# Performance work log

Measured on AMD Instinct MI355X. Metric: run time of the kernel, lower is better.

The kernel has to match this reference:

```python
import jax, jax.numpy as jnp
import numpy as np

EPS = 1e-7


def setup_inputs() -> dict:
    key = jax.random.key(0)
    k1, k2, k3 = jax.random.split(key, 3)
    B, Nt, Nv, D = 64, 128, 256, 512
    text_feats = jax.random.normal(k1, (B, Nt, D), dtype=jnp.float32)
    visual_feats = jax.random.normal(k2, (B, Nv, D), dtype=jnp.float32)
    attention_mask = jax.random.randint(k3, (B, Nt), 0, 2, dtype=jnp.int32)
    return {"text_feats": text_feats, "visual_feats": visual_feats,
            "attention_mask": attention_mask}


def _l2norm(x):
    return x / jnp.clip(jnp.linalg.norm(x, axis=-1, keepdims=True), 1e-12)


def reference(text_feats, visual_feats, attention_mask):
    # Normalize token features (F.normalize along D)
    t = _l2norm(text_feats)            # (B, Nt, D)
    v = _l2norm(visual_feats)          # (B, Nv, D)
    # All-pairs token similarities: (B, B, Nt, Nv)
    token_sims = jnp.einsum('itd,jvd->ijtv', t, v)
    # Max over visual tokens -> (B, B, Nt)
    max_sims = jnp.max(token_sims, axis=3)
    # Masked mean over text tokens -> (B, B)
    mask = attention_mask.astype(jnp.float32)[:, None, :]   # (B, 1, Nt) broadcasts over pairs
    masked_sum = jnp.sum(max_sims * mask, axis=2)            # (B, B)
    valid = jnp.clip(jnp.sum(mask, axis=2), EPS)             # (B, 1)
    clip_sims = masked_sum / valid                           # (B, B)
    # Symmetric InfoNCE on the diagonal
    B = clip_sims.shape[0]
    diag = jnp.arange(B)
    losses_t2v = -jax.nn.log_softmax(clip_sims, axis=1)[diag, diag]
    losses_v2t = -jax.nn.log_softmax(clip_sims.T, axis=1)[diag, diag]
    contrastive_loss = jnp.mean(losses_t2v + losses_v2t) / 2.0
    # Regularization: keep negative token sims near zero
    neg_sims = jnp.clip(token_sims, -20.0, 0.0)
    reg_loss = 0.15 * jnp.mean(neg_sims ** 2)
    return contrastive_loss + reg_loss
```

## Files before the change

### kernel.cpp

```cpp
#include <hip/hip_runtime.h>
#include <hip/hip_bf16.h>

#define BB 64
#define NT 128
#define NV 256
#define DD 512
#define BKB 128
#define EPSF 1e-7f

typedef __attribute__((ext_vector_type(8))) int i32x8;
typedef __attribute__((ext_vector_type(4))) int i32x4;
typedef __attribute__((ext_vector_type(4))) float f32x4;

__device__ __forceinline__ void glds16(const uchar* g, uchar* l) {
    __builtin_amdgcn_global_load_lds(
        (const __attribute__((address_space(1))) unsigned int*)g,
        (__attribute__((address_space(3))) unsigned int*)l, 16, 0, 0);
}

__global__ __launch_bounds__(256) void k_normalize(
    const float* __restrict__ tf, const float* __restrict__ vf,
    uchar* __restrict__ tn, uchar* __restrict__ vn,
    float* __restrict__ reg_sum) {
    if (blockIdx.x == 0 && threadIdx.x == 0) *reg_sum = 0.0f;
    const int w = threadIdx.x >> 6, l = threadIdx.x & 63;
    const int row = blockIdx.x * 4 + w;
    const float* src;
    uchar* dst;
    if (row < BB * NT) {
        src = tf + (size_t)row * DD;
        dst = tn + (size_t)row * DD;
    } else {
        int r = row - BB * NT;
        src = vf + (size_t)r * DD;
        dst = vn + (size_t)r * DD;
    }
    float4 x0 = ((const float4*)src)[l * 2];
    float4 x1 = ((const float4*)src)[l * 2 + 1];
    float ss = x0.x * x0.x + x0.y * x0.y + x0.z * x0.z + x0.w * x0.w
             + x1.x * x1.x + x1.y * x1.y + x1.z * x1.z + x1.w * x1.w;
    #pragma unroll
    for (int off = 32; off; off >>= 1) ss += __shfl_xor(ss, off, 64);
    float scale = 1.0f / fmaxf(sqrtf(ss), 1e-12f);
    int p0 = __builtin_amdgcn_cvt_pk_fp8_f32(x0.x * scale, x0.y * scale, 0, 0);
    p0 = __builtin_amdgcn_cvt_pk_fp8_f32(x0.z * scale, x0.w * scale, p0, 1);
    int p1 = __builtin_amdgcn_cvt_pk_fp8_f32(x1.x * scale, x1.y * scale, 0, 0);
    p1 = __builtin_amdgcn_cvt_pk_fp8_f32(x1.z * scale, x1.w * scale, p1, 1);
    ((uint2*)dst)[l] = make_uint2((unsigned)p0, (unsigned)p1);
}

__global__ __launch_bounds__(512, 2) void k_gemm(
    const uchar* __restrict__ tn, const uchar* __restrict__ vn,
    const int* __restrict__ mask,
    float* __restrict__ clip_sims, float* __restrict__ reg_sum) {
    __shared__ uchar sT0[NT * BKB];
    __shared__ uchar sT1[NT * BKB];
    __shared__ uchar sV0[NV * BKB];
    __shared__ uchar sV1[NV * BKB];
    __shared__ float maxbuf[NT][4];
    __shared__ float redw[8];
    __shared__ float c0[2], c1[2];

    const int i = blockIdx.x, j = blockIdx.y;
    const int tid = threadIdx.x;
    const int l = tid & 63, w = tid >> 6;
    const int wr = w >> 2, wc = w & 3;
    const int m15 = l & 15, q = l >> 4;

    const uchar* tbase = tn + (size_t)i * NT * DD;
    const uchar* vbase = vn + (size_t)j * NV * DD;

    int t_off[2], v_off[4];
    #pragma unroll
    for (int s = 0; s < 2; ++s) {
        int f = s * 512 + tid;
        int r = f >> 3, p = f & 7, g = (p - r) & 7;
        t_off[s] = r * DD + g * 16;
    }
    #pragma unroll
    for (int s = 0; s < 4; ++s) {
        int f = s * 512 + tid;
        int r = f >> 3, p = f & 7, g = (p - r) & 7;
        v_off[s] = r * DD + g * 16;
    }

    int a_b0[4], a_b1[4], b_b0[4], b_b1[4];
    #pragma unroll
    for (int rt = 0; rt < 4; ++rt) {
        int row = wr * 64 + rt * 16 + m15;
        a_b0[rt] = row * BKB + (((2 * q + row) & 7) * 16);
        a_b1[rt] = row * BKB + (((2 * q + 1 + row) & 7) * 16);
    }
    #pragma unroll
    for (int ct = 0; ct < 4; ++ct) {
        int row = wc * 64 + ct * 16 + m15;
        b_b0[ct] = row * BKB + (((2 * q + row) & 7) * 16);
        b_b1[ct] = row * BKB + (((2 * q + 1 + row) & 7) * 16);
    }

    f32x4 acc[4][4];
    #pragma unroll
    for (int rt = 0; rt < 4; ++rt)
        #pragma unroll
        for (int ct = 0; ct < 4; ++ct) acc[rt][ct] = (f32x4){0.f, 0.f, 0.f, 0.f};

    auto stage = [&](uchar* dT, uchar* dV, int kk) {
        #pragma unroll
        for (int s = 0; s < 2; ++s)
            glds16(tbase + t_off[s] + kk, dT + (s * 512 + tid) * 16);
        #pragma unroll
        for (int s = 0; s < 4; ++s)
            glds16(vbase + v_off[s] + kk, dV + (s * 512 + tid) * 16);
    };
    auto compute = [&](const uchar* bT, const uchar* bV) {
        i32x8 bf[4];
        #pragma unroll
        for (int ct = 0; ct < 4; ++ct) {
            i32x4 lo = *(const i32x4*)(bV + b_b0[ct]);
            i32x4 hi = *(const i32x4*)(bV + b_b1[ct]);
            bf[ct] = (i32x8){lo.x, lo.y, lo.z, lo.w, hi.x, hi.y, hi.z, hi.w};
        }
        #pragma unroll
        for (int rt = 0; rt < 4; ++rt) {
            i32x4 lo = *(const i32x4*)(bT + a_b0[rt]);
            i32x4 hi = *(const i32x4*)(bT + a_b1[rt]);
            i32x8 a = (i32x8){lo.x, lo.y, lo.z, lo.w, hi.x, hi.y, hi.z, hi.w};
            #pragma unroll
            for (int ct = 0; ct < 4; ++ct)
                acc[rt][ct] = __builtin_amdgcn_mfma_scale_f32_16x16x128_f8f6f4(
                    a, bf[ct], acc[rt][ct],
                    0 , 0 ,
                    0, 127 , 0, 127 );
        }
    };

    stage(sT0, sV0, 0);
    stage(sT1, sV1, 1 * BKB);

    asm volatile("s_waitcnt vmcnt(6)" ::: "memory");
    __builtin_amdgcn_s_barrier();
    asm volatile("" ::: "memory");
    compute(sT0, sV0);
    asm volatile("" ::: "memory");
    __builtin_amdgcn_s_barrier();
    stage(sT0, sV0, 2 * BKB);

    asm volatile("s_waitcnt vmcnt(6)" ::: "memory");
    __builtin_amdgcn_s_barrier();
    asm volatile("" ::: "memory");
    compute(sT1, sV1);
    asm volatile("" ::: "memory");
    __builtin_amdgcn_s_barrier();
    stage(sT1, sV1, 3 * BKB);

    asm volatile("s_waitcnt vmcnt(6)" ::: "memory");
    __builtin_amdgcn_s_barrier();
    asm volatile("" ::: "memory");
    compute(sT0, sV0);
    asm volatile("" ::: "memory");
    __builtin_amdgcn_s_barrier();

    asm volatile("s_waitcnt vmcnt(0)" ::: "memory");
    __builtin_amdgcn_s_barrier();
    asm volatile("" ::: "memory");
    compute(sT1, sV1);

    float rp = 0.0f;
    #pragma unroll
    for (int rt = 0; rt < 4; ++rt)
        #pragma unroll
        for (int ct = 0; ct < 4; ++ct)
            #pragma unroll
            for (int r = 0; r < 4; ++r) {
                float m = fminf(acc[rt][ct][r], 0.0f);
                rp = fmaf(m, m, rp);
            }

    #pragma unroll
    for (int rt = 0; rt < 4; ++rt)
        #pragma unroll
        for (int r = 0; r < 4; ++r) {
            float m = acc[rt][0][r];
            #pragma unroll
            for (int ct = 1; ct < 4; ++ct) m = fmaxf(m, acc[rt][ct][r]);
            #pragma unroll
            for (int msk = 1; msk < 16; msk <<= 1)
                m = fmaxf(m, __shfl_xor(m, msk, 64));
            if (m15 == 0)
                maxbuf[wr * 64 + rt * 16 + q * 4 + r][wc] = m;
        }

    #pragma unroll
    for (int off = 32; off; off >>= 1) rp += __shfl_down(rp, off, 64);
    if (l == 0) redw[w] = rp;
    __syncthreads();

    if (tid < NT) {
        float rm = fmaxf(fmaxf(maxbuf[tid][0], maxbuf[tid][1]),
                         fmaxf(maxbuf[tid][2], maxbuf[tid][3]));
        float mf = (float)mask[i * NT + tid];
        float v = rm * mf;
        #pragma unroll
        for (int off = 32; off; off >>= 1) {
            v += __shfl_down(v, off, 64);
            mf += __shfl_down(mf, off, 64);
        }
        if (l == 0) { c0[w] = v; c1[w] = mf; }
    }
    __syncthreads();
    if (tid == 0) {
        clip_sims[i * BB + j] = (c0[0] + c0[1]) / fmaxf(c1[0] + c1[1], EPSF);
        float s = 0.0f;
        #pragma unroll
        for (int x = 0; x < 8; ++x) s += redw[x];
        atomicAdd(reg_sum, s);
    }
}

__global__ __launch_bounds__(256) void k_loss(
    const float* __restrict__ clip_sims, const float* __restrict__ reg_sum,
    float* __restrict__ out) {
    __shared__ float sc[BB][BB + 1];
    __shared__ float lrow[BB], lcol[BB];
    int tid = threadIdx.x;
    for (int idx = tid; idx < BB * BB; idx += 256)
        sc[idx / BB][idx % BB] = clip_sims[idx];
    __syncthreads();
    if (tid < BB) {
        int i = tid;
        float m = sc[i][0];
        #pragma unroll
        for (int j = 1; j < BB; ++j) m = fmaxf(m, sc[i][j]);
        float s = 0.0f;
        #pragma unroll
        for (int j = 0; j < BB; ++j) s += expf(sc[i][j] - m);
        lrow[i] = m + logf(s) - sc[i][i];
    } else if (tid < 2 * BB) {
        int i = tid - BB;
        float m = sc[0][i];
        #pragma unroll
        for (int j = 1; j < BB; ++j) m = fmaxf(m, sc[j][i]);
        float s = 0.0f;
        #pragma unroll
        for (int j = 0; j < BB; ++j) s += expf(sc[j][i] - m);
        lcol[i] = m + logf(s) - sc[i][i];
    }
    __syncthreads();
    if (tid == 0) {
        float tot = 0.0f;
        for (int i = 0; i < BB; ++i) tot += lrow[i] + lcol[i];
        float contrastive = tot / (2.0f * BB);
        double denom = (double)BB * BB * NT * NV;
        float reg = 0.15f * (float)((double)reg_sum[0] / denom);
        out[0] = contrastive + reg;
    }
}

extern "C" void kernel_launch(void* const* d_in, const int* in_sizes, int n_in,
                              void* d_out, int out_size, void* d_ws, size_t ws_size,
                              hipStream_t stream) {
    const float* tf = (const float*)d_in[0];
    const float* vf = (const float*)d_in[1];
    const int* mask = (const int*)d_in[2];
    float* out = (float*)d_out;

    char* ws = (char*)d_ws;
    size_t tn_bytes = (size_t)BB * NT * DD;
    size_t vn_bytes = (size_t)BB * NV * DD;
    size_t cs_bytes = (size_t)BB * BB * sizeof(float);

    uchar* tn = (uchar*)ws;
    uchar* vn = (uchar*)(ws + tn_bytes);
    float* clip_sims = (float*)(ws + tn_bytes + vn_bytes);
    float* reg_sum = (float*)(ws + tn_bytes + vn_bytes + cs_bytes);

    k_normalize<<<(BB * NT + BB * NV) / 4, 256, 0, stream>>>(tf, vf, tn, vn, reg_sum);
    k_gemm<<<dim3(BB, BB), 512, 0, stream>>>(tn, vn, mask, clip_sims, reg_sum);
    k_loss<<<1, 256, 0, stream>>>(clip_sims, reg_sum, out);
}
```

Before: 230.4 us.

## Single-buffer visual tile in LDS so two GEMM blocks fit per CU

```diff
diff --git a/kernel.cpp b/kernel.cpp
--- a/kernel.cpp
+++ b/kernel.cpp
@@ -55,8 +55,7 @@
     float* __restrict__ clip_sims, float* __restrict__ reg_sum) {
     __shared__ uchar sT0[NT * BKB];
     __shared__ uchar sT1[NT * BKB];
-    __shared__ uchar sV0[NV * BKB];
-    __shared__ uchar sV1[NV * BKB];
+    __shared__ uchar sV[NV * BKB];
     __shared__ float maxbuf[NT][4];
     __shared__ float redw[8];
     __shared__ float c0[2], c1[2];
@@ -104,20 +103,22 @@
         #pragma unroll
         for (int ct = 0; ct < 4; ++ct) acc[rt][ct] = (f32x4){0.f, 0.f, 0.f, 0.f};
 
-    auto stage = [&](uchar* dT, uchar* dV, int kk) {
+    auto stageV = [&](int kk) {
+        #pragma unroll
+        for (int s = 0; s < 4; ++s)
+            glds16(vbase + v_off[s] + kk, sV + (s * 512 + tid) * 16);
+    };
+    auto stageT = [&](uchar* dT, int kk) {
         #pragma unroll
         for (int s = 0; s < 2; ++s)
             glds16(tbase + t_off[s] + kk, dT + (s * 512 + tid) * 16);
-        #pragma unroll
-        for (int s = 0; s < 4; ++s)
-            glds16(vbase + v_off[s] + kk, dV + (s * 512 + tid) * 16);
     };
-    auto compute = [&](const uchar* bT, const uchar* bV) {
+    auto compute = [&](const uchar* bT) {
         i32x8 bf[4];
         #pragma unroll
         for (int ct = 0; ct < 4; ++ct) {
-            i32x4 lo = *(const i32x4*)(bV + b_b0[ct]);
-            i32x4 hi = *(const i32x4*)(bV + b_b1[ct]);
+            i32x4 lo = *(const i32x4*)(sV + b_b0[ct]);
+            i32x4 hi = *(const i32x4*)(sV + b_b1[ct]);
             bf[ct] = (i32x8){lo.x, lo.y, lo.z, lo.w, hi.x, hi.y, hi.z, hi.w};
         }
         #pragma unroll
@@ -134,36 +135,40 @@
         }
     };
 
-    stage(sT0, sV0, 0);
-    stage(sT1, sV1, 1 * BKB);
-
-    asm volatile("s_waitcnt vmcnt(6)" ::: "memory");
-    __builtin_amdgcn_s_barrier();
-    asm volatile("" ::: "memory");
-    compute(sT0, sV0);
-    asm volatile("" ::: "memory");
-    __builtin_amdgcn_s_barrier();
-    stage(sT0, sV0, 2 * BKB);
-
-    asm volatile("s_waitcnt vmcnt(6)" ::: "memory");
-    __builtin_amdgcn_s_barrier();
-    asm volatile("" ::: "memory");
-    compute(sT1, sV1);
-    asm volatile("" ::: "memory");
-    __builtin_amdgcn_s_barrier();
-    stage(sT1, sV1, 3 * BKB);
-
-    asm volatile("s_waitcnt vmcnt(6)" ::: "memory");
-    __builtin_amdgcn_s_barrier();
-    asm volatile("" ::: "memory");
-    compute(sT0, sV0);
-    asm volatile("" ::: "memory");
-    __builtin_amdgcn_s_barrier();
+    stageV(0);
+    stageT(sT0, 0);
+    stageT(sT1, 1 * BKB);
+
+    asm volatile("s_waitcnt vmcnt(2)" ::: "memory");
+    __builtin_amdgcn_s_barrier();
+    asm volatile("" ::: "memory");
+    compute(sT0);
+    asm volatile("" ::: "memory");
+    __builtin_amdgcn_s_barrier();
+    stageV(1 * BKB);
+    stageT(sT0, 2 * BKB);
+
+    asm volatile("s_waitcnt vmcnt(2)" ::: "memory");
+    __builtin_amdgcn_s_barrier();
+    asm volatile("" ::: "memory");
+    compute(sT1);
+    asm volatile("" ::: "memory");
+    __builtin_amdgcn_s_barrier();
+    stageV(2 * BKB);
+    stageT(sT1, 3 * BKB);
+
+    asm volatile("s_waitcnt vmcnt(2)" ::: "memory");
+    __builtin_amdgcn_s_barrier();
+    asm volatile("" ::: "memory");
+    compute(sT0);
+    asm volatile("" ::: "memory");
+    __builtin_amdgcn_s_barrier();
+    stageV(3 * BKB);
 
     asm volatile("s_waitcnt vmcnt(0)" ::: "memory");
     __builtin_amdgcn_s_barrier();
     asm volatile("" ::: "memory");
-    compute(sT1, sV1);
+    compute(sT1);
 
     float rp = 0.0f;
     #pragma unroll
```

New measurement: 242.8 us. +5.4%, slower.

## Keep text tile resident in LDS and loop over four visual batches per block

Applied to the files above, without the earlier changes.

```diff
diff --git a/kernel.cpp b/kernel.cpp
--- a/kernel.cpp
+++ b/kernel.cpp
@@ -53,22 +53,21 @@
     const uchar* __restrict__ tn, const uchar* __restrict__ vn,
     const int* __restrict__ mask,
     float* __restrict__ clip_sims, float* __restrict__ reg_sum) {
-    __shared__ uchar sT0[NT * BKB];
-    __shared__ uchar sT1[NT * BKB];
+    __shared__ uchar sT[4][NT * BKB];
     __shared__ uchar sV0[NV * BKB];
     __shared__ uchar sV1[NV * BKB];
     __shared__ float maxbuf[NT][4];
     __shared__ float redw[8];
     __shared__ float c0[2], c1[2];
 
-    const int i = blockIdx.x, j = blockIdx.y;
+    const int i = blockIdx.x;
+    const int j0 = blockIdx.y * 4;
     const int tid = threadIdx.x;
     const int l = tid & 63, w = tid >> 6;
     const int wr = w >> 2, wc = w & 3;
     const int m15 = l & 15, q = l >> 4;
 
     const uchar* tbase = tn + (size_t)i * NT * DD;
-    const uchar* vbase = vn + (size_t)j * NV * DD;
 
     int t_off[2], v_off[4];
     #pragma unroll
@@ -99,18 +98,12 @@
     }
 
     f32x4 acc[4][4];
-    #pragma unroll
-    for (int rt = 0; rt < 4; ++rt)
-        #pragma unroll
-        for (int ct = 0; ct < 4; ++ct) acc[rt][ct] = (f32x4){0.f, 0.f, 0.f, 0.f};
-
-    auto stage = [&](uchar* dT, uchar* dV, int kk) {
-        #pragma unroll
-        for (int s = 0; s < 2; ++s)
-            glds16(tbase + t_off[s] + kk, dT + (s * 512 + tid) * 16);
+    float rp = 0.0f;
+
+    auto stageV = [&](uchar* dV, const uchar* vb, int kk) {
         #pragma unroll
         for (int s = 0; s < 4; ++s)
-            glds16(vbase + v_off[s] + kk, dV + (s * 512 + tid) * 16);
+            glds16(vb + v_off[s] + kk, dV + (s * 512 + tid) * 16);
     };
     auto compute = [&](const uchar* bT, const uchar* bV) {
         i32x8 bf[4];
@@ -134,82 +127,91 @@
         }
     };
 
-    stage(sT0, sV0, 0);
-    stage(sT1, sV1, 1 * BKB);
-
-    asm volatile("s_waitcnt vmcnt(6)" ::: "memory");
-    __builtin_amdgcn_s_barrier();
-    asm volatile("" ::: "memory");
-    compute(sT0, sV0);
-    asm volatile("" ::: "memory");
-    __builtin_amdgcn_s_barrier();
-    stage(sT0, sV0, 2 * BKB);
-
-    asm volatile("s_waitcnt vmcnt(6)" ::: "memory");
-    __builtin_amdgcn_s_barrier();
-    asm volatile("" ::: "memory");
-    compute(sT1, sV1);
-    asm volatile("" ::: "memory");
-    __builtin_amdgcn_s_barrier();
-    stage(sT1, sV1, 3 * BKB);
-
-    asm volatile("s_waitcnt vmcnt(6)" ::: "memory");
-    __builtin_amdgcn_s_barrier();
-    asm volatile("" ::: "memory");
-    compute(sT0, sV0);
-    asm volatile("" ::: "memory");
-    __builtin_amdgcn_s_barrier();
-
-    asm volatile("s_waitcnt vmcnt(0)" ::: "memory");
-    __builtin_amdgcn_s_barrier();
-    asm volatile("" ::: "memory");
-    compute(sT1, sV1);
-
-    float rp = 0.0f;
-    #pragma unroll
-    for (int rt = 0; rt < 4; ++rt)
-        #pragma unroll
-        for (int ct = 0; ct < 4; ++ct)
+    #pragma unroll
+    for (int c = 0; c < 4; ++c)
+        #pragma unroll
+        for (int s = 0; s < 2; ++s)
+            glds16(tbase + t_off[s] + c * BKB, sT[c] + (s * 512 + tid) * 16);
+    {
+        const uchar* vb = vn + (size_t)j0 * NV * DD;
+        stageV(sV0, vb, 0);
+        stageV(sV1, vb, BKB);
+    }
+
+    #pragma unroll
+    for (int jj = 0; jj < 4; ++jj) {
+        #pragma unroll
+        for (int rt = 0; rt < 4; ++rt)
+            #pragma unroll
+            for (int ct = 0; ct < 4; ++ct) acc[rt][ct] = (f32x4){0.f, 0.f, 0.f, 0.f};
+
+        #pragma unroll
+        for (int k = 0; k < 4; ++k) {
+            const int m = jj * 4 + k;
+            if (m < 15) { asm volatile("s_waitcnt vmcnt(4)" ::: "memory"); }
+            else        { asm volatile("s_waitcnt vmcnt(0)" ::: "memory"); }
+            __builtin_amdgcn_s_barrier();
+            asm volatile("" ::: "memory");
+            compute(sT[k], (m & 1) ? sV1 : sV0);
+            asm volatile("" ::: "memory");
+            __builtin_amdgcn_s_barrier();
+            const int mn = m + 2;
+            if (mn < 16) {
+                const uchar* vb = vn + (size_t)(j0 + (mn >> 2)) * NV * DD;
+                stageV((mn & 1) ? sV1 : sV0, vb, (mn & 3) * BKB);
+            }
+        }
+
+        #pragma unroll
+        for (int rt = 0; rt < 4; ++rt)
+            #pragma unroll
+            for (int ct = 0; ct < 4; ++ct)
+                #pragma unroll
+                for (int r = 0; r < 4; ++r) {
+                    float m = fminf(acc[rt][ct][r], 0.0f);
+                    rp = fmaf(m, m, rp);
+                }
+        #pragma unroll
+        for (int rt = 0; rt < 4; ++rt)
             #pragma unroll
             for (int r = 0; r < 4; ++r) {
-                float m = fminf(acc[rt][ct][r], 0.0f);
-                rp = fmaf(m, m, rp);
+                float m = acc[rt][0][r];
+                #pragma unroll
+                for (int ct = 1; ct < 4; ++ct) m = fmaxf(m, acc[rt][ct][r]);
+                #pragma unroll
+                for (int msk = 1; msk < 16; msk <<= 1)
+                    m = fmaxf(m, __shfl_xor(m, msk, 64));
+                if (m15 == 0)
+                    maxbuf[wr * 64 + rt * 16 + q * 4 + r][wc] = m;
             }
-
-    #pragma unroll
-    for (int rt = 0; rt < 4; ++rt)
-        #pragma unroll
-        for (int r = 0; r < 4; ++r) {
-            float m = acc[rt][0][r];
-            #pragma unroll
-            for (int ct = 1; ct < 4; ++ct) m = fmaxf(m, acc[rt][ct][r]);
-            #pragma unroll
-            for (int msk = 1; msk < 16; msk <<= 1)
-                m = fmaxf(m, __shfl_xor(m, msk, 64));
-            if (m15 == 0)
-                maxbuf[wr * 64 + rt * 16 + q * 4 + r][wc] = m;
-        }
+        asm volatile("s_waitcnt lgkmcnt(0)" ::: "memory");
+        __builtin_amdgcn_s_barrier();
+        asm volatile("" ::: "memory");
+        if (tid < NT) {
+            float rm = fmaxf(fmaxf(maxbuf[tid][0], maxbuf[tid][1]),
+                             fmaxf(maxbuf[tid][2], maxbuf[tid][3]));
+            float mf = (float)mask[i * NT + tid];
+            float v = rm * mf;
+            #pragma unroll
+            for (int off = 32; off; off >>= 1) {
+                v += __shfl_down(v, off, 64);
+                mf += __shfl_down(mf, off, 64);
+            }
+            if (l == 0) { c0[w] = v; c1[w] = mf; }
+        }
+        asm volatile("s_waitcnt lgkmcnt(0)" ::: "memory");
+        __builtin_amdgcn_s_barrier();
+        asm volatile("" ::: "memory");
+        if (tid == 0)
+            clip_sims[i * BB + j0 + jj] =
+                (c0[0] + c0[1]) / fmaxf(c1[0] + c1[1], EPSF);
+    }
 
     #pragma unroll
     for (int off = 32; off; off >>= 1) rp += __shfl_down(rp, off, 64);
     if (l == 0) redw[w] = rp;
     __syncthreads();
-
-    if (tid < NT) {
-        float rm = fmaxf(fmaxf(maxbuf[tid][0], maxbuf[tid][1]),
-                         fmaxf(maxbuf[tid][2], maxbuf[tid][3]));
-        float mf = (float)mask[i * NT + tid];
-        float v = rm * mf;
-        #pragma unroll
-        for (int off = 32; off; off >>= 1) {
-            v += __shfl_down(v, off, 64);
-            mf += __shfl_down(mf, off, 64);
-        }
-        if (l == 0) { c0[w] = v; c1[w] = mf; }
-    }
-    __syncthreads();
     if (tid == 0) {
-        clip_sims[i * BB + j] = (c0[0] + c0[1]) / fmaxf(c1[0] + c1[1], EPSF);
         float s = 0.0f;
         #pragma unroll
         for (int x = 0; x < 8; ++x) s += redw[x];
@@ -275,6 +277,6 @@
     float* reg_sum = (float*)(ws + tn_bytes + vn_bytes + cs_bytes);
 
     k_normalize<<<(BB * NT + BB * NV) / 4, 256, 0, stream>>>(tf, vf, tn, vn, reg_sum);
-    k_gemm<<<dim3(BB, BB), 512, 0, stream>>>(tn, vn, mask, clip_sims, reg_sum);
+    k_gemm<<<dim3(BB, BB / 4), 512, 0, stream>>>(tn, vn, mask, clip_sims, reg_sum);
     k_loss<<<1, 256, 0, stream>>>(clip_sims, reg_sum, out);
 }
```

Result: slower. 526.2 us (+128.3%).

## Split GEMM blocks over text-row halves and combine pair sums atomically

Applied to the files above, without the earlier changes.

```diff
diff --git a/kernel.cpp b/kernel.cpp
--- a/kernel.cpp
+++ b/kernel.cpp
@@ -21,8 +21,14 @@
 __global__ __launch_bounds__(256) void k_normalize(
     const float* __restrict__ tf, const float* __restrict__ vf,
     uchar* __restrict__ tn, uchar* __restrict__ vn,
+    float* __restrict__ cs_num, float* __restrict__ cs_den,
     float* __restrict__ reg_sum) {
     if (blockIdx.x == 0 && threadIdx.x == 0) *reg_sum = 0.0f;
+    if (blockIdx.x < 16) {
+        int idx = blockIdx.x * 256 + threadIdx.x;
+        cs_num[idx] = 0.0f;
+        cs_den[idx] = 0.0f;
+    }
     const int w = threadIdx.x >> 6, l = threadIdx.x & 63;
     const int row = blockIdx.x * 4 + w;
     const float* src;
@@ -49,45 +55,34 @@
     ((uint2*)dst)[l] = make_uint2((unsigned)p0, (unsigned)p1);
 }
 
-__global__ __launch_bounds__(512, 2) void k_gemm(
+__global__ __launch_bounds__(256, 2) void k_gemm(
     const uchar* __restrict__ tn, const uchar* __restrict__ vn,
     const int* __restrict__ mask,
-    float* __restrict__ clip_sims, float* __restrict__ reg_sum) {
-    __shared__ uchar sT0[NT * BKB];
-    __shared__ uchar sT1[NT * BKB];
+    float* __restrict__ cs_num, float* __restrict__ cs_den,
+    float* __restrict__ reg_sum) {
+    __shared__ uchar sTT[64 * BKB];
     __shared__ uchar sV0[NV * BKB];
     __shared__ uchar sV1[NV * BKB];
-    __shared__ float maxbuf[NT][4];
-    __shared__ float redw[8];
-    __shared__ float c0[2], c1[2];
-
-    const int i = blockIdx.x, j = blockIdx.y;
+    __shared__ float maxbuf[64][4];
+    __shared__ float redw[4];
+
+    const int i = blockIdx.x >> 1, h = blockIdx.x & 1;
+    const int j = blockIdx.y;
     const int tid = threadIdx.x;
     const int l = tid & 63, w = tid >> 6;
-    const int wr = w >> 2, wc = w & 3;
+    const int wc = w;
     const int m15 = l & 15, q = l >> 4;
 
-    const uchar* tbase = tn + (size_t)i * NT * DD;
+    const uchar* tbase = tn + ((size_t)i * NT + h * 64) * DD;
     const uchar* vbase = vn + (size_t)j * NV * DD;
 
-    int t_off[2], v_off[4];
-    #pragma unroll
-    for (int s = 0; s < 2; ++s) {
-        int f = s * 512 + tid;
-        int r = f >> 3, p = f & 7, g = (p - r) & 7;
-        t_off[s] = r * DD + g * 16;
-    }
-    #pragma unroll
-    for (int s = 0; s < 4; ++s) {
-        int f = s * 512 + tid;
-        int r = f >> 3, p = f & 7, g = (p - r) & 7;
-        v_off[s] = r * DD + g * 16;
-    }
+    const int sbase = (tid >> 3) * DD + ((((tid & 7) - (tid >> 3)) & 7) * 16);
+    const int ldst = tid * 16;
 
     int a_b0[4], a_b1[4], b_b0[4], b_b1[4];
     #pragma unroll
     for (int rt = 0; rt < 4; ++rt) {
-        int row = wr * 64 + rt * 16 + m15;
+        int row = rt * 16 + m15;
         a_b0[rt] = row * BKB + (((2 * q + row) & 7) * 16);
         a_b1[rt] = row * BKB + (((2 * q + 1 + row) & 7) * 16);
     }
@@ -104,15 +99,17 @@
         #pragma unroll
         for (int ct = 0; ct < 4; ++ct) acc[rt][ct] = (f32x4){0.f, 0.f, 0.f, 0.f};
 
-    auto stage = [&](uchar* dT, uchar* dV, int kk) {
+    auto stageT = [&](int kk) {
         #pragma unroll
         for (int s = 0; s < 2; ++s)
-            glds16(tbase + t_off[s] + kk, dT + (s * 512 + tid) * 16);
-        #pragma unroll
-        for (int s = 0; s < 4; ++s)
-            glds16(vbase + v_off[s] + kk, dV + (s * 512 + tid) * 16);
+            glds16(tbase + sbase + s * 16384 + kk, sTT + s * 4096 + ldst);
     };
-    auto compute = [&](const uchar* bT, const uchar* bV) {
+    auto stageV = [&](uchar* dV, int kk) {
+        #pragma unroll
+        for (int s = 0; s < 8; ++s)
+            glds16(vbase + sbase + s * 16384 + kk, dV + s * 4096 + ldst);
+    };
+    auto compute = [&](const uchar* bV) {
         i32x8 bf[4];
         #pragma unroll
         for (int ct = 0; ct < 4; ++ct) {
@@ -122,8 +119,8 @@
         }
         #pragma unroll
         for (int rt = 0; rt < 4; ++rt) {
-            i32x4 lo = *(const i32x4*)(bT + a_b0[rt]);
-            i32x4 hi = *(const i32x4*)(bT + a_b1[rt]);
+            i32x4 lo = *(const i32x4*)(sTT + a_b0[rt]);
+            i32x4 hi = *(const i32x4*)(sTT + a_b1[rt]);
             i32x8 a = (i32x8){lo.x, lo.y, lo.z, lo.w, hi.x, hi.y, hi.z, hi.w};
             #pragma unroll
             for (int ct = 0; ct < 4; ++ct)
@@ -134,36 +131,40 @@
         }
     };
 
-    stage(sT0, sV0, 0);
-    stage(sT1, sV1, 1 * BKB);
-
-    asm volatile("s_waitcnt vmcnt(6)" ::: "memory");
-    __builtin_amdgcn_s_barrier();
-    asm volatile("" ::: "memory");
-    compute(sT0, sV0);
-    asm volatile("" ::: "memory");
-    __builtin_amdgcn_s_barrier();
-    stage(sT0, sV0, 2 * BKB);
-
-    asm volatile("s_waitcnt vmcnt(6)" ::: "memory");
-    __builtin_amdgcn_s_barrier();
-    asm volatile("" ::: "memory");
-    compute(sT1, sV1);
-    asm volatile("" ::: "memory");
-    __builtin_amdgcn_s_barrier();
-    stage(sT1, sV1, 3 * BKB);
-
-    asm volatile("s_waitcnt vmcnt(6)" ::: "memory");
-    __builtin_amdgcn_s_barrier();
-    asm volatile("" ::: "memory");
-    compute(sT0, sV0);
-    asm volatile("" ::: "memory");
-    __builtin_amdgcn_s_barrier();
+    stageT(0);
+    stageV(sV0, 0);
+    stageV(sV1, 1 * BKB);
+
+    asm volatile("s_waitcnt vmcnt(8)" ::: "memory");
+    __builtin_amdgcn_s_barrier();
+    asm volatile("" ::: "memory");
+    compute(sV0);
+    asm volatile("" ::: "memory");
+    __builtin_amdgcn_s_barrier();
+    stageT(1 * BKB);
+    stageV(sV0, 2 * BKB);
+
+    asm volatile("s_waitcnt vmcnt(8)" ::: "memory");
+    __builtin_amdgcn_s_barrier();
+    asm volatile("" ::: "memory");
+    compute(sV1);
+    asm volatile("" ::: "memory");
+    __builtin_amdgcn_s_barrier();
+    stageT(2 * BKB);
+    stageV(sV1, 3 * BKB);
+
+    asm volatile("s_waitcnt vmcnt(8)" ::: "memory");
+    __builtin_amdgcn_s_barrier();
+    asm volatile("" ::: "memory");
+    compute(sV0);
+    asm volatile("" ::: "memory");
+    __builtin_amdgcn_s_barrier();
+    stageT(3 * BKB);
 
     asm volatile("s_waitcnt vmcnt(0)" ::: "memory");
     __builtin_amdgcn_s_barrier();
     asm volatile("" ::: "memory");
-    compute(sT1, sV1);
+    compute(sV1);
 
     float rp = 0.0f;
     #pragma unroll
@@ -187,7 +188,7 @@
             for (int msk = 1; msk < 16; msk <<= 1)
                 m = fmaxf(m, __shfl_xor(m, msk, 64));
             if (m15 == 0)
-                maxbuf[wr * 64 + rt * 16 + q * 4 + r][wc] = m;
+                maxbuf[rt * 16 + q * 4 + r][wc] = m;
         }
 
     #pragma unroll
@@ -195,36 +196,32 @@
     if (l == 0) redw[w] = rp;
     __syncthreads();
 
-    if (tid < NT) {
+    if (tid < 64) {
         float rm = fmaxf(fmaxf(maxbuf[tid][0], maxbuf[tid][1]),
                          fmaxf(maxbuf[tid][2], maxbuf[tid][3]));
-        float mf = (float)mask[i * NT + tid];
+        float mf = (float)mask[i * NT + h * 64 + tid];
         float v = rm * mf;
         #pragma unroll
         for (int off = 32; off; off >>= 1) {
             v += __shfl_down(v, off, 64);
             mf += __shfl_down(mf, off, 64);
         }
-        if (l == 0) { c0[w] = v; c1[w] = mf; }
-    }
-    __syncthreads();
-    if (tid == 0) {
-        clip_sims[i * BB + j] = (c0[0] + c0[1]) / fmaxf(c1[0] + c1[1], EPSF);
-        float s = 0.0f;
-        #pragma unroll
-        for (int x = 0; x < 8; ++x) s += redw[x];
-        atomicAdd(reg_sum, s);
+        if (tid == 0) {
+            atomicAdd(cs_num + i * BB + j, v);
+            atomicAdd(cs_den + i * BB + j, mf);
+            atomicAdd(reg_sum, redw[0] + redw[1] + redw[2] + redw[3]);
+        }
     }
 }
 
 __global__ __launch_bounds__(256) void k_loss(
-    const float* __restrict__ clip_sims, const float* __restrict__ reg_sum,
-    float* __restrict__ out) {
+    const float* __restrict__ cs_num, const float* __restrict__ cs_den,
+    const float* __restrict__ reg_sum, float* __restrict__ out) {
     __shared__ float sc[BB][BB + 1];
     __shared__ float lrow[BB], lcol[BB];
     int tid = threadIdx.x;
     for (int idx = tid; idx < BB * BB; idx += 256)
-        sc[idx / BB][idx % BB] = clip_sims[idx];
+        sc[idx / BB][idx % BB] = cs_num[idx] / fmaxf(cs_den[idx], EPSF);
     __syncthreads();
     if (tid < BB) {
         int i = tid;
@@ -271,10 +268,13 @@
 
     uchar* tn = (uchar*)ws;
     uchar* vn = (uchar*)(ws + tn_bytes);
-    float* clip_sims = (float*)(ws + tn_bytes + vn_bytes);
-    float* reg_sum = (float*)(ws + tn_bytes + vn_bytes + cs_bytes);
-
-    k_normalize<<<(BB * NT + BB * NV) / 4, 256, 0, stream>>>(tf, vf, tn, vn, reg_sum);
-    k_gemm<<<dim3(BB, BB), 512, 0, stream>>>(tn, vn, mask, clip_sims, reg_sum);
-    k_loss<<<1, 256, 0, stream>>>(clip_sims, reg_sum, out);
-}
+    float* cs_num = (float*)(ws + tn_bytes + vn_bytes);
+    float* cs_den = (float*)(ws + tn_bytes + vn_bytes + cs_bytes);
+    float* reg_sum = (float*)(ws + tn_bytes + vn_bytes + 2 * cs_bytes);
+
+    k_normalize<<<(BB * NT + BB * NV) / 4, 256, 0, stream>>>(
+        tf, vf, tn, vn, cs_num, cs_den, reg_sum);
+    k_gemm<<<dim3(BB * 2, BB), 256, 0, stream>>>(
+        tn, vn, mask, cs_num, cs_den, reg_sum);
+    k_loss<<<1, 256, 0, stream>>>(cs_num, cs_den, reg_sum, out);
+}
```

Measured after the change: 239.7 us. +4.0%, slower.
